# Kernel tuning notes

Hardware: AMD Instinct MI355X
Metric: run time of the kernel (lower is better)

The kernel has to match this reference:

```python
import jax, jax.numpy as jnp
import numpy as np

B = 262144      # batch
DIN = 100       # input covariate dim (cfg_density[0][0])
H = 64          # hidden dim
G = 10          # num_grid -> density output dim G+1
NH = 5          # number of dosage-bucket heads in Multi_head


def setup_inputs() -> dict:
    key = jax.random.key(0)
    ks = jax.random.split(key, 16)
    s = 0.05
    return {
        "dosage": jax.random.uniform(ks[0], (B,), dtype=jnp.float32),
        "x": jax.random.normal(ks[1], (B, DIN), dtype=jnp.float32),
        # density feature MLP (two Linear+ReLU layers)
        "dW0": jax.random.normal(ks[2], (DIN, H), dtype=jnp.float32) * s,
        "db0": jax.random.normal(ks[3], (H,), dtype=jnp.float32) * s,
        "dW1": jax.random.normal(ks[4], (H, H), dtype=jnp.float32) * s,
        "db1": jax.random.normal(ks[5], (H,), dtype=jnp.float32) * s,
        # Density_Block: Linear(H -> G+1) then softmax + grid interpolation
        "dbW": jax.random.normal(ks[6], (H, G + 1), dtype=jnp.float32) * s,
        "dbB": jax.random.normal(ks[7], (G + 1,), dtype=jnp.float32) * s,
        # Multi_head: 5 structurally identical heads, params stacked on axis 0
        # layer0: Treat_Linear(64 -> 64, relu, istreat=1)
        "W0": jax.random.normal(ks[8], (NH, H, H), dtype=jnp.float32) * s,
        "tw0": jax.random.normal(ks[9], (NH, H), dtype=jnp.float32) * s,
        "b0": jax.random.normal(ks[10], (NH, H), dtype=jnp.float32) * s,
        # layer1 (last): Treat_Linear(64 -> 1, no act, istreat=1)
        "W1": jax.random.normal(ks[11], (NH, H, 1), dtype=jnp.float32) * s,
        "tw1": jax.random.normal(ks[12], (NH, 1), dtype=jnp.float32) * s,
        "b1": jax.random.normal(ks[13], (NH, 1), dtype=jnp.float32) * s,
    }


def reference(dosage, x, dW0, db0, dW1, db1, dbW, dbB, W0, tw0, b0, W1, tw1, b1):
    # hidden feature MLP
    hidden = jax.nn.relu(x @ dW0 + db0)
    hidden = jax.nn.relu(hidden @ dW1 + db1)            # [B, H]

    # ---- Density_Block: softmax over grid, dual gather + linear interpolation
    p = jax.nn.softmax(hidden @ dbW + dbB, axis=1)      # [B, G+1]
    tB = dosage * G
    U = jnp.ceil(tB)
    inter = 1.0 - (U - tB)                              # fractional position in cell
    Ui = U.astype(jnp.int32)
    Li = Ui - 1
    Li = Li + (Li < 0).astype(jnp.int32)                # clamp L=-1 -> 0
    pL = jnp.take_along_axis(p, Li[:, None], axis=1)[:, 0]
    pU = jnp.take_along_axis(p, Ui[:, None], axis=1)[:, 0]
    g = pL + (pU - pL) * inter                          # [B]

    # ---- Multi_head: 5 heads on dosage buckets [0,.2),[.2,.4),...,[.8,1.)
    t = dosage
    # layer0: out = feat @ W + t * tw + b, relu; compute all heads, select later
    h0 = jax.nn.relu(
        jnp.einsum('bi,hio->bho', hidden, W0)
        + t[:, None, None] * tw0[None]
        + b0[None]
    )                                                   # [B, NH, H]
    # last layer: no activation
    out1 = (jnp.einsum('bho,hoj->bhj', h0, W1)
            + t[:, None, None] * tw1[None]
            + b1[None])                                 # [B, NH, 1]
    bucket = jnp.clip(jnp.floor(t * NH).astype(jnp.int32), 0, NH - 1)
    Q = jnp.take_along_axis(out1, bucket[:, None, None], axis=1)[:, 0, :]  # [B, 1]
    return g, Q
```

## Files before the change

kernel.cpp:

```cpp
#include <hip/hip_runtime.h>

typedef __attribute__((ext_vector_type(8))) short  short8;
typedef __attribute__((ext_vector_type(4))) float  floatx4;
typedef __attribute__((ext_vector_type(4))) int    intx4;

constexpr int DIN = 100;
constexpr int H   = 64;
constexpr int G   = 10;
constexpr int NH  = 5;
constexpr int MWG = 128;
constexpr int HP  = 72;
constexpr int PBP = 20;

constexpr int NF_DW0 = 16, NF_DW1 = 8, NF_DBW = 2;
constexpr int NF_LIN = NF_DW0 + NF_DW1 + NF_DBW;
constexpr int NF_TOT = NF_LIN + 40;

__device__ __forceinline__ unsigned short f2bf_rne(float f) {
    union { float f; unsigned u; } v{f};
    unsigned r = v.u + 0x7FFF + ((v.u >> 16) & 1);
    return (unsigned short)(r >> 16);
}

__device__ __forceinline__ short8 pack8(const float* f) {
    intx4 p;
    #pragma unroll
    for (int j = 0; j < 4; ++j) {
        unsigned a = __float_as_uint(f[2 * j])     + 0x8000u;
        unsigned b = __float_as_uint(f[2 * j + 1]) + 0x8000u;
        p[j] = (int)((b & 0xFFFF0000u) | (a >> 16));
    }
    union { intx4 i; short8 s; } u; u.i = p;
    return u.s;
}

__device__ __forceinline__ unsigned pack2bf(float a, float b) {
    unsigned ua = __float_as_uint(a) + 0x8000u;
    unsigned ub = __float_as_uint(b) + 0x8000u;
    return (ua >> 16) | (ub & 0xFFFF0000u);
}

__device__ __forceinline__ short8 ldfrag(const unsigned short* __restrict__ ws,
                                         int f, int lane) {
    return *(const short8*)(ws + (size_t)(f * 64 + lane) * 8);
}

__global__ __launch_bounds__(64) void pack_kernel(
    const float* __restrict__ dW0, const float* __restrict__ dW1,
    const float* __restrict__ dbW, const float* __restrict__ W0,
    unsigned short* __restrict__ ws)
{
    const int f = blockIdx.x;
    const int lane = threadIdx.x;
    const int q = lane >> 4, cl = lane & 15;
    float v[8];
    if (f < NF_DW0) {
        int c = f >> 2, g = f & 3;
        #pragma unroll
        for (int j = 0; j < 8; ++j) {
            int k = c * 32 + q * 8 + j, n = g * 16 + cl;
            v[j] = (k < DIN) ? dW0[k * H + n] : 0.0f;
        }
    } else if (f < NF_DW0 + NF_DW1) {
        int r = f - NF_DW0; int c = r >> 2, g = r & 3;
        #pragma unroll
        for (int j = 0; j < 8; ++j) {
            int k = c * 32 + q * 8 + j, n = g * 16 + cl;
            v[j] = dW1[k * H + n];
        }
    } else if (f < NF_LIN) {
        int c = f - (NF_DW0 + NF_DW1);
        #pragma unroll
        for (int j = 0; j < 8; ++j) {
            int k = c * 32 + q * 8 + j, n = cl;
            v[j] = (n <= G) ? dbW[k * (G + 1) + n] : 0.0f;
        }
    } else {
        int r = f - NF_LIN; int h = r >> 3; r &= 7; int c = r >> 2, g = r & 3;
        #pragma unroll
        for (int j = 0; j < 8; ++j) {
            int k = c * 32 + q * 8 + j, n = g * 16 + cl;
            v[j] = W0[(h * H + k) * H + n];
        }
    }
    short8 s;
    #pragma unroll
    for (int j = 0; j < 8; ++j) s[j] = (short)f2bf_rne(v[j]);
    *(short8*)(ws + (size_t)(f * 64 + lane) * 8) = s;
}

__global__ __launch_bounds__(256, 3) void drnet_mfma(
    const float* __restrict__ dosage, const float* __restrict__ x,
    const float* __restrict__ db0, const float* __restrict__ db1,
    const float* __restrict__ dbB,
    const float* __restrict__ tw0, const float* __restrict__ b0,
    const float* __restrict__ W1, const float* __restrict__ tw1,
    const float* __restrict__ b1,
    const unsigned short* __restrict__ wsfrag,
    float* __restrict__ outg, float* __restrict__ outq)
{
    __shared__ unsigned short hbuf[MWG * HP];
    __shared__ float          pbuf[4][16][PBP];
    __shared__ int            perm[MWG];
    __shared__ float          tbuf[MWG];
    __shared__ unsigned char  bkbuf[MWG];
    __shared__ float          qbuf[MWG];
    __shared__ int            hist[NH];
    __shared__ int            offs[NH];

    const int tid  = threadIdx.x;
    const int wave = tid >> 6, lane = tid & 63;
    const int q = lane >> 4, cl = lane & 15;
    const int rowbase = blockIdx.x * MWG + wave * 32;
    unsigned short* hb = hbuf + wave * 32 * HP;

    if (tid < NH) hist[tid] = 0;
    __syncthreads();
    {
        float t8[2][4];
        int   bk8[2][4];
        #pragma unroll
        for (int mt = 0; mt < 2; ++mt) {
            floatx4 tv = *(const floatx4*)(dosage + rowbase + mt * 16 + 4 * q);
            #pragma unroll
            for (int r = 0; r < 4; ++r) {
                float t = tv[r];
                t8[mt][r] = t;
                int bk = (int)floorf(t * (float)NH);
                bk8[mt][r] = min(max(bk, 0), NH - 1);
            }
        }
        if (cl == 0) {
            #pragma unroll
            for (int mt = 0; mt < 2; ++mt)
                #pragma unroll
                for (int r = 0; r < 4; ++r)
                    atomicAdd(&hist[bk8[mt][r]], 1);
        }
        __syncthreads();
        if (tid == 0) {
            int a = 0;
            #pragma unroll
            for (int h = 0; h < NH; ++h) { offs[h] = a; a += hist[h]; }
        }
        __syncthreads();
        if (cl == 0) {
            #pragma unroll
            for (int mt = 0; mt < 2; ++mt)
                #pragma unroll
                for (int r = 0; r < 4; ++r) {
                    const int bk  = bk8[mt][r];
                    const int pos = atomicAdd(&offs[bk], 1);
                    perm[pos]  = wave * 32 + mt * 16 + 4 * q + r;
                    tbuf[pos]  = t8[mt][r];
                    bkbuf[pos] = (unsigned char)bk;
                }
        }
    }

    #pragma unroll 1
    for (int mt = 0; mt < 2; ++mt) {
        short8 a1[4];
        const float* xr = x + (size_t)(rowbase + mt * 16 + cl) * DIN;
        #pragma unroll
        for (int cch = 0; cch < 4; ++cch) {
            float f[8];
            if (cch < 3) {
                floatx4 u0 = *(const floatx4*)(xr + cch * 32 + q * 8);
                floatx4 u1 = *(const floatx4*)(xr + cch * 32 + q * 8 + 4);
                f[0]=u0.x; f[1]=u0.y; f[2]=u0.z; f[3]=u0.w;
                f[4]=u1.x; f[5]=u1.y; f[6]=u1.z; f[7]=u1.w;
            } else {
                if (q == 0) {
                    floatx4 u0 = *(const floatx4*)(xr + 96);
                    f[0]=u0.x; f[1]=u0.y; f[2]=u0.z; f[3]=u0.w;
                    f[4]=f[5]=f[6]=f[7]=0.0f;
                } else {
                    #pragma unroll
                    for (int j = 0; j < 8; ++j) f[j] = 0.0f;
                }
            }
            a1[cch] = pack8(f);
        }
        floatx4 acc[4];
        #pragma unroll
        for (int g = 0; g < 4; ++g) acc[g] = (floatx4)0.0f;
        #pragma unroll
        for (int cch = 0; cch < 4; ++cch)
            #pragma unroll
            for (int g = 0; g < 4; ++g) {
                short8 bf = ldfrag(wsfrag, cch * 4 + g, lane);
                acc[g] = __builtin_amdgcn_mfma_f32_16x16x32_bf16(bf, a1[cch], acc[g], 0, 0, 0);
            }
        #pragma unroll
        for (int g = 0; g < 4; ++g) {
            floatx4 bias = *(const floatx4*)(db0 + g * 16 + 4 * q);
            float v0 = fmaxf(acc[g][0] + bias[0], 0.0f);
            float v1 = fmaxf(acc[g][1] + bias[1], 0.0f);
            float v2 = fmaxf(acc[g][2] + bias[2], 0.0f);
            float v3 = fmaxf(acc[g][3] + bias[3], 0.0f);
            *(uint2*)(hb + (size_t)(mt * 16 + cl) * HP + g * 16 + 4 * q) =
                make_uint2(pack2bf(v0, v1), pack2bf(v2, v3));
        }
    }

    #pragma unroll 1
    for (int mt = 0; mt < 2; ++mt) {
        short8 a2[2];
        #pragma unroll
        for (int cch = 0; cch < 2; ++cch)
            a2[cch] = *(const short8*)(hb + (mt * 16 + cl) * HP + cch * 32 + q * 8);
        floatx4 acc[4];
        #pragma unroll
        for (int g = 0; g < 4; ++g) acc[g] = (floatx4)0.0f;
        #pragma unroll
        for (int cch = 0; cch < 2; ++cch)
            #pragma unroll
            for (int g = 0; g < 4; ++g) {
                short8 bf = ldfrag(wsfrag, NF_DW0 + cch * 4 + g, lane);
                acc[g] = __builtin_amdgcn_mfma_f32_16x16x32_bf16(bf, a2[cch], acc[g], 0, 0, 0);
            }
        #pragma unroll
        for (int g = 0; g < 4; ++g) {
            floatx4 bias = *(const floatx4*)(db1 + g * 16 + 4 * q);
            float v0 = fmaxf(acc[g][0] + bias[0], 0.0f);
            float v1 = fmaxf(acc[g][1] + bias[1], 0.0f);
            float v2 = fmaxf(acc[g][2] + bias[2], 0.0f);
            float v3 = fmaxf(acc[g][3] + bias[3], 0.0f);
            *(uint2*)(hb + (size_t)(mt * 16 + cl) * HP + g * 16 + 4 * q) =
                make_uint2(pack2bf(v0, v1), pack2bf(v2, v3));
        }
    }

    short8 af[2][2];
    #pragma unroll
    for (int mt = 0; mt < 2; ++mt)
        #pragma unroll
        for (int cch = 0; cch < 2; ++cch)
            af[mt][cch] = *(const short8*)(hb + (mt * 16 + cl) * HP + cch * 32 + q * 8);

    {
        floatx4 accd[2];
        accd[0] = (floatx4)0.0f; accd[1] = (floatx4)0.0f;
        #pragma unroll
        for (int cch = 0; cch < 2; ++cch) {
            short8 bf = ldfrag(wsfrag, NF_DW0 + NF_DW1 + cch, lane);
            #pragma unroll
            for (int mt = 0; mt < 2; ++mt)
                accd[mt] = __builtin_amdgcn_mfma_f32_16x16x32_bf16(bf, af[mt][cch], accd[mt], 0, 0, 0);
        }
        #pragma unroll
        for (int mt = 0; mt < 2; ++mt) {
            floatx4 ev;
            float sp = 0.0f;
            #pragma unroll
            for (int r = 0; r < 4; ++r) {
                const int gd = 4 * q + r;
                float e = (gd <= G) ? __expf(accd[mt][r] + dbB[gd]) : 0.0f;
                ev[r] = e;
                sp += e;
            }
            float s = sp;
            s += __shfl_xor(s, 16); s += __shfl_xor(s, 32);
            *(floatx4*)(&pbuf[wave][cl][4 * q]) = ev;
            const float t  = dosage[rowbase + mt * 16 + cl];
            const float tB = t * (float)G;
            const float U  = ceilf(tB);
            const float inter = 1.0f - (U - tB);
            int Ui = (int)U; int Li = Ui - 1; if (Li < 0) Li = 0;
            const float pL = pbuf[wave][cl][Li];
            const float pU = pbuf[wave][cl][Ui];
            if (q == 0)
                outg[rowbase + mt * 16 + cl] = (pL + (pU - pL) * inter) / s;
        }
    }

    __syncthreads();
    #pragma unroll 1
    for (int mt = 0; mt < 2; ++mt) {
        const int base = (wave * 2 + mt) * 16;
        const int prow = perm[base + cl];
        short8 ag[2];
        ag[0] = *(const short8*)(hbuf + prow * HP + q * 8);
        ag[1] = *(const short8*)(hbuf + prow * HP + 32 + q * 8);
        const float tme  = tbuf[base + cl];
        const int   bkme = bkbuf[base + cl];
        const int   blo  = bkbuf[base], bhi = bkbuf[base + 15];
        float qp = 0.0f;
        #pragma unroll 1
        for (int h = blo; h <= bhi; ++h) {
            floatx4 acch[4];
            #pragma unroll
            for (int g = 0; g < 4; ++g) acch[g] = (floatx4)0.0f;
            #pragma unroll
            for (int cch = 0; cch < 2; ++cch)
                #pragma unroll
                for (int g = 0; g < 4; ++g) {
                    short8 bf = ldfrag(wsfrag, NF_LIN + h * 8 + cch * 4 + g, lane);
                    acch[g] = __builtin_amdgcn_mfma_f32_16x16x32_bf16(bf, ag[cch], acch[g], 0, 0, 0);
                }
            if (bkme == h) {
                #pragma unroll
                for (int g = 0; g < 4; ++g) {
                    const int off = h * H + g * 16 + 4 * q;
                    floatx4 tw0v = *(const floatx4*)(tw0 + off);
                    floatx4 b0v  = *(const floatx4*)(b0  + off);
                    floatx4 w1v  = *(const floatx4*)(W1  + off);
                    #pragma unroll
                    for (int r = 0; r < 4; ++r)
                        qp += fmaxf(acch[g][r] + tme * tw0v[r] + b0v[r], 0.0f) * w1v[r];
                }
            }
        }
        qp += __shfl_xor(qp, 16); qp += __shfl_xor(qp, 32);
        if (q == 0)
            qbuf[prow] = qp + tme * tw1[bkme] + b1[bkme];
    }

    __syncthreads();
    if (tid < MWG / 4) {
        floatx4 v = *(const floatx4*)(qbuf + tid * 4);
        *(floatx4*)(outq + blockIdx.x * MWG + tid * 4) = v;
    }
}

extern "C" void kernel_launch(void* const* d_in, const int* in_sizes, int n_in,
                              void* d_out, int out_size, void* d_ws, size_t ws_size,
                              hipStream_t stream) {
    const float* dosage = (const float*)d_in[0];
    const float* x      = (const float*)d_in[1];
    const float* dW0    = (const float*)d_in[2];
    const float* db0    = (const float*)d_in[3];
    const float* dW1    = (const float*)d_in[4];
    const float* db1    = (const float*)d_in[5];
    const float* dbW    = (const float*)d_in[6];
    const float* dbB    = (const float*)d_in[7];
    const float* W0     = (const float*)d_in[8];
    const float* tw0    = (const float*)d_in[9];
    const float* b0     = (const float*)d_in[10];
    const float* W1     = (const float*)d_in[11];
    const float* tw1    = (const float*)d_in[12];
    const float* b1     = (const float*)d_in[13];

    const int Btot = in_sizes[0];
    float* outg = (float*)d_out;
    float* outq = outg + Btot;
    unsigned short* ws = (unsigned short*)d_ws;

    pack_kernel<<<NF_TOT, 64, 0, stream>>>(dW0, dW1, dbW, W0, ws);
    drnet_mfma<<<Btot / MWG, 256, 0, stream>>>(dosage, x, db0, db1, dbB,
                                               tw0, b0, W1, tw1, b1,
                                               ws, outg, outq);
}
```

Before: 204.7 us.

## Prefetch x and dosage before the histogram barriers and interleave both M-tiles

Global loads of x rows and dosage are issued at the top of the kernel, before the bucket-sort histogram. The barriers there are replaced with LDS-only waits (lgkmcnt) so those loads stay in flight across the sort. The two 16-row tiles in each GEMM layer are fully unrolled and their MFMAs interleaved, sharing each weight fragment load and giving more independent MFMA chains. The cost is much higher register pressure from 14 floatx4 of x per lane plus doubled accumulators, which could lower occupancy or cause spills.

```diff
diff --git a/kernel.cpp b/kernel.cpp
--- a/kernel.cpp
+++ b/kernel.cpp
@@ -43,6 +43,12 @@
 __device__ __forceinline__ short8 ldfrag(const unsigned short* __restrict__ ws,
                                          int f, int lane) {
     return *(const short8*)(ws + (size_t)(f * 64 + lane) * 8);
+}
+
+__device__ __forceinline__ void bar_lgkm() {
+    asm volatile("s_waitcnt lgkmcnt(0)" ::: "memory");
+    __builtin_amdgcn_s_barrier();
+    asm volatile("" ::: "memory");
 }
 
 __global__ __launch_bounds__(64) void pack_kernel(
@@ -114,22 +120,36 @@
     const int rowbase = blockIdx.x * MWG + wave * 32;
     unsigned short* hb = hbuf + wave * 32 * HP;
 
+    floatx4 tvs[2];
+    #pragma unroll
+    for (int mt = 0; mt < 2; ++mt)
+        tvs[mt] = *(const floatx4*)(dosage + rowbase + mt * 16 + 4 * q);
+    floatx4 xv[2][7];
+    #pragma unroll
+    for (int mt = 0; mt < 2; ++mt) {
+        const float* xr = x + (size_t)(rowbase + mt * 16 + cl) * DIN;
+        #pragma unroll
+        for (int cch = 0; cch < 3; ++cch) {
+            xv[mt][2 * cch]     = *(const floatx4*)(xr + cch * 32 + q * 8);
+            xv[mt][2 * cch + 1] = *(const floatx4*)(xr + cch * 32 + q * 8 + 4);
+        }
+        xv[mt][6] = (q == 0) ? *(const floatx4*)(xr + 96) : (floatx4)0.0f;
+    }
+
     if (tid < NH) hist[tid] = 0;
-    __syncthreads();
+    bar_lgkm();
     {
         float t8[2][4];
         int   bk8[2][4];
         #pragma unroll
-        for (int mt = 0; mt < 2; ++mt) {
-            floatx4 tv = *(const floatx4*)(dosage + rowbase + mt * 16 + 4 * q);
+        for (int mt = 0; mt < 2; ++mt)
             #pragma unroll
             for (int r = 0; r < 4; ++r) {
-                float t = tv[r];
+                float t = tvs[mt][r];
                 t8[mt][r] = t;
                 int bk = (int)floorf(t * (float)NH);
                 bk8[mt][r] = min(max(bk, 0), NH - 1);
             }
-        }
         if (cl == 0) {
             #pragma unroll
             for (int mt = 0; mt < 2; ++mt)
@@ -137,13 +157,13 @@
                 for (int r = 0; r < 4; ++r)
                     atomicAdd(&hist[bk8[mt][r]], 1);
         }
-        __syncthreads();
+        bar_lgkm();
         if (tid == 0) {
             int a = 0;
             #pragma unroll
             for (int h = 0; h < NH; ++h) { offs[h] = a; a += hist[h]; }
         }
-        __syncthreads();
+        bar_lgkm();
         if (cl == 0) {
             #pragma unroll
             for (int mt = 0; mt < 2; ++mt)
@@ -158,88 +178,100 @@
         }
     }
 
-    #pragma unroll 1
-    for (int mt = 0; mt < 2; ++mt) {
-        short8 a1[4];
-        const float* xr = x + (size_t)(rowbase + mt * 16 + cl) * DIN;
-        #pragma unroll
-        for (int cch = 0; cch < 4; ++cch) {
-            float f[8];
-            if (cch < 3) {
-                floatx4 u0 = *(const floatx4*)(xr + cch * 32 + q * 8);
-                floatx4 u1 = *(const floatx4*)(xr + cch * 32 + q * 8 + 4);
-                f[0]=u0.x; f[1]=u0.y; f[2]=u0.z; f[3]=u0.w;
-                f[4]=u1.x; f[5]=u1.y; f[6]=u1.z; f[7]=u1.w;
-            } else {
-                if (q == 0) {
-                    floatx4 u0 = *(const floatx4*)(xr + 96);
-                    f[0]=u0.x; f[1]=u0.y; f[2]=u0.z; f[3]=u0.w;
-                    f[4]=f[5]=f[6]=f[7]=0.0f;
+    {
+        short8 a1[2][4];
+        #pragma unroll
+        for (int mt = 0; mt < 2; ++mt)
+            #pragma unroll
+            for (int cch = 0; cch < 4; ++cch) {
+                float f[8];
+                if (cch < 3) {
+                    #pragma unroll
+                    for (int j = 0; j < 4; ++j) {
+                        f[j]     = xv[mt][2 * cch][j];
+                        f[4 + j] = xv[mt][2 * cch + 1][j];
+                    }
                 } else {
                     #pragma unroll
-                    for (int j = 0; j < 8; ++j) f[j] = 0.0f;
+                    for (int j = 0; j < 4; ++j) {
+                        f[j]     = xv[mt][6][j];
+                        f[4 + j] = 0.0f;
+                    }
                 }
-            }
-            a1[cch] = pack8(f);
-        }
-        floatx4 acc[4];
-        #pragma unroll
-        for (int g = 0; g < 4; ++g) acc[g] = (floatx4)0.0f;
+                a1[mt][cch] = pack8(f);
+            }
+        floatx4 acc[2][4];
+        #pragma unroll
+        for (int mt = 0; mt < 2; ++mt)
+            #pragma unroll
+            for (int g = 0; g < 4; ++g) acc[mt][g] = (floatx4)0.0f;
         #pragma unroll
         for (int cch = 0; cch < 4; ++cch)
             #pragma unroll
             for (int g = 0; g < 4; ++g) {
                 short8 bf = ldfrag(wsfrag, cch * 4 + g, lane);
-                acc[g] = __builtin_amdgcn_mfma_f32_16x16x32_bf16(bf, a1[cch], acc[g], 0, 0, 0);
-            }
-        #pragma unroll
-        for (int g = 0; g < 4; ++g) {
-            floatx4 bias = *(const floatx4*)(db0 + g * 16 + 4 * q);
-            float v0 = fmaxf(acc[g][0] + bias[0], 0.0f);
-            float v1 = fmaxf(acc[g][1] + bias[1], 0.0f);
-            float v2 = fmaxf(acc[g][2] + bias[2], 0.0f);
-            float v3 = fmaxf(acc[g][3] + bias[3], 0.0f);
-            *(uint2*)(hb + (size_t)(mt * 16 + cl) * HP + g * 16 + 4 * q) =
-                make_uint2(pack2bf(v0, v1), pack2bf(v2, v3));
-        }
-    }
-
-    #pragma unroll 1
-    for (int mt = 0; mt < 2; ++mt) {
-        short8 a2[2];
-        #pragma unroll
-        for (int cch = 0; cch < 2; ++cch)
-            a2[cch] = *(const short8*)(hb + (mt * 16 + cl) * HP + cch * 32 + q * 8);
-        floatx4 acc[4];
-        #pragma unroll
-        for (int g = 0; g < 4; ++g) acc[g] = (floatx4)0.0f;
+                acc[0][g] = __builtin_amdgcn_mfma_f32_16x16x32_bf16(bf, a1[0][cch], acc[0][g], 0, 0, 0);
+                acc[1][g] = __builtin_amdgcn_mfma_f32_16x16x32_bf16(bf, a1[1][cch], acc[1][g], 0, 0, 0);
+            }
+        #pragma unroll
+        for (int mt = 0; mt < 2; ++mt)
+            #pragma unroll
+            for (int g = 0; g < 4; ++g) {
+                floatx4 bias = *(const floatx4*)(db0 + g * 16 + 4 * q);
+                float v0 = fmaxf(acc[mt][g][0] + bias[0], 0.0f);
+                float v1 = fmaxf(acc[mt][g][1] + bias[1], 0.0f);
+                float v2 = fmaxf(acc[mt][g][2] + bias[2], 0.0f);
+                float v3 = fmaxf(acc[mt][g][3] + bias[3], 0.0f);
+                *(uint2*)(hb + (size_t)(mt * 16 + cl) * HP + g * 16 + 4 * q) =
+                    make_uint2(pack2bf(v0, v1), pack2bf(v2, v3));
+            }
+    }
+
+    {
+        short8 a2[2][2];
+        #pragma unroll
+        for (int mt = 0; mt < 2; ++mt)
+            #pragma unroll
+            for (int cch = 0; cch < 2; ++cch)
+                a2[mt][cch] = *(const short8*)(hb + (mt * 16 + cl) * HP + cch * 32 + q * 8);
+        floatx4 acc[2][4];
+        #pragma unroll
+        for (int mt = 0; mt < 2; ++mt)
+            #pragma unroll
+            for (int g = 0; g < 4; ++g) acc[mt][g] = (floatx4)0.0f;
         #pragma unroll
         for (int cch = 0; cch < 2; ++cch)
             #pragma unroll
             for (int g = 0; g < 4; ++g) {
                 short8 bf = ldfrag(wsfrag, NF_DW0 + cch * 4 + g, lane);
-                acc[g] = __builtin_amdgcn_mfma_f32_16x16x32_bf16(bf, a2[cch], acc[g], 0, 0, 0);
-            }
-        #pragma unroll
-        for (int g = 0; g < 4; ++g) {
-            floatx4 bias = *(const floatx4*)(db1 + g * 16 + 4 * q);
-            float v0 = fmaxf(acc[g][0] + bias[0], 0.0f);
-            float v1 = fmaxf(acc[g][1] + bias[1], 0.0f);
-            float v2 = fmaxf(acc[g][2] + bias[2], 0.0f);
-            float v3 = fmaxf(acc[g][3] + bias[3], 0.0f);
-            *(uint2*)(hb + (size_t)(mt * 16 + cl) * HP + g * 16 + 4 * q) =
-                make_uint2(pack2bf(v0, v1), pack2bf(v2, v3));
-        }
-    }
-
-    short8 af[2][2];
-    #pragma unroll
-    for (int mt = 0; mt < 2; ++mt)
-        #pragma unroll
-        for (int cch = 0; cch < 2; ++cch)
-            af[mt][cch] = *(const short8*)(hb + (mt * 16 + cl) * HP + cch * 32 + q * 8);
-
-    {
+                acc[0][g] = __builtin_amdgcn_mfma_f32_16x16x32_bf16(bf, a2[0][cch], acc[0][g], 0, 0, 0);
+                acc[1][g] = __builtin_amdgcn_mfma_f32_16x16x32_bf16(bf, a2[1][cch], acc[1][g], 0, 0, 0);
+            }
+        #pragma unroll
+        for (int mt = 0; mt < 2; ++mt)
+            #pragma unroll
+            for (int g = 0; g < 4; ++g) {
+                floatx4 bias = *(const floatx4*)(db1 + g * 16 + 4 * q);
+                float v0 = fmaxf(acc[mt][g][0] + bias[0], 0.0f);
+                float v1 = fmaxf(acc[mt][g][1] + bias[1], 0.0f);
+                float v2 = fmaxf(acc[mt][g][2] + bias[2], 0.0f);
+                float v3 = fmaxf(acc[mt][g][3] + bias[3], 0.0f);
+                *(uint2*)(hb + (size_t)(mt * 16 + cl) * HP + g * 16 + 4 * q) =
+                    make_uint2(pack2bf(v0, v1), pack2bf(v2, v3));
+            }
+    }
+
+    {
+        float tden[2];
+        #pragma unroll
+        for (int mt = 0; mt < 2; ++mt)
+            tden[mt] = dosage[rowbase + mt * 16 + cl];
+        short8 af[2][2];
+        #pragma unroll
+        for (int mt = 0; mt < 2; ++mt)
+            #pragma unroll
+            for (int cch = 0; cch < 2; ++cch)
+                af[mt][cch] = *(const short8*)(hb + (mt * 16 + cl) * HP + cch * 32 + q * 8);
         floatx4 accd[2];
         accd[0] = (floatx4)0.0f; accd[1] = (floatx4)0.0f;
         #pragma unroll
@@ -263,7 +295,7 @@
             float s = sp;
             s += __shfl_xor(s, 16); s += __shfl_xor(s, 32);
             *(floatx4*)(&pbuf[wave][cl][4 * q]) = ev;
-            const float t  = dosage[rowbase + mt * 16 + cl];
+            const float t  = tden[mt];
             const float tB = t * (float)G;
             const float U  = ceilf(tB);
             const float inter = 1.0f - (U - tB);
@@ -276,45 +308,53 @@
     }
 
     __syncthreads();
-    #pragma unroll 1
-    for (int mt = 0; mt < 2; ++mt) {
-        const int base = (wave * 2 + mt) * 16;
-        const int prow = perm[base + cl];
-        short8 ag[2];
-        ag[0] = *(const short8*)(hbuf + prow * HP + q * 8);
-        ag[1] = *(const short8*)(hbuf + prow * HP + 32 + q * 8);
-        const float tme  = tbuf[base + cl];
-        const int   bkme = bkbuf[base + cl];
-        const int   blo  = bkbuf[base], bhi = bkbuf[base + 15];
-        float qp = 0.0f;
-        #pragma unroll 1
-        for (int h = blo; h <= bhi; ++h) {
-            floatx4 acch[4];
-            #pragma unroll
-            for (int g = 0; g < 4; ++g) acch[g] = (floatx4)0.0f;
-            #pragma unroll
-            for (int cch = 0; cch < 2; ++cch)
+    {
+        short8 ag[2][2];
+        int    prow[2], bkme[2], blo[2], bhi[2];
+        float  tme[2];
+        #pragma unroll
+        for (int mt = 0; mt < 2; ++mt) {
+            const int base = (wave * 2 + mt) * 16;
+            prow[mt] = perm[base + cl];
+            ag[mt][0] = *(const short8*)(hbuf + prow[mt] * HP + q * 8);
+            ag[mt][1] = *(const short8*)(hbuf + prow[mt] * HP + 32 + q * 8);
+            tme[mt]  = tbuf[base + cl];
+            bkme[mt] = bkbuf[base + cl];
+            blo[mt]  = bkbuf[base];
+            bhi[mt]  = bkbuf[base + 15];
+        }
+        #pragma unroll
+        for (int mt = 0; mt < 2; ++mt) {
+            float qp = 0.0f;
+            #pragma unroll 1
+            for (int h = blo[mt]; h <= bhi[mt]; ++h) {
+                floatx4 acch[4];
                 #pragma unroll
-                for (int g = 0; g < 4; ++g) {
-                    short8 bf = ldfrag(wsfrag, NF_LIN + h * 8 + cch * 4 + g, lane);
-                    acch[g] = __builtin_amdgcn_mfma_f32_16x16x32_bf16(bf, ag[cch], acch[g], 0, 0, 0);
+                for (int g = 0; g < 4; ++g) acch[g] = (floatx4)0.0f;
+                #pragma unroll
+                for (int cch = 0; cch < 2; ++cch)
+                    #pragma unroll
+                    for (int g = 0; g < 4; ++g) {
+                        short8 bf = ldfrag(wsfrag, NF_LIN + h * 8 + cch * 4 + g, lane);
+                        acch[g] = __builtin_amdgcn_mfma_f32_16x16x32_bf16(bf, ag[mt][cch], acch[g], 0, 0, 0);
+                    }
+                if (bkme[mt] == h) {
+                    #pragma unroll
+                    for (int g = 0; g < 4; ++g) {
+                        const int off = h * H + g * 16 + 4 * q;
+                        floatx4 tw0v = *(const floatx4*)(tw0 + off);
+                        floatx4 b0v  = *(const floatx4*)(b0  + off);
+                        floatx4 w1v  = *(const floatx4*)(W1  + off);
+                        #pragma unroll
+                        for (int r = 0; r < 4; ++r)
+                            qp += fmaxf(acch[g][r] + tme[mt] * tw0v[r] + b0v[r], 0.0f) * w1v[r];
+                    }
                 }
-            if (bkme == h) {
-                #pragma unroll
-                for (int g = 0; g < 4; ++g) {
-                    const int off = h * H + g * 16 + 4 * q;
-                    floatx4 tw0v = *(const floatx4*)(tw0 + off);
-                    floatx4 b0v  = *(const floatx4*)(b0  + off);
-                    floatx4 w1v  = *(const floatx4*)(W1  + off);
-                    #pragma unroll
-                    for (int r = 0; r < 4; ++r)
-                        qp += fmaxf(acch[g][r] + tme * tw0v[r] + b0v[r], 0.0f) * w1v[r];
-                }
-            }
-        }
-        qp += __shfl_xor(qp, 16); qp += __shfl_xor(qp, 32);
-        if (q == 0)
-            qbuf[prow] = qp + tme * tw1[bkme] + b1[bkme];
+            }
+            qp += __shfl_xor(qp, 16); qp += __shfl_xor(qp, 32);
+            if (q == 0)
+                qbuf[prow[mt]] = qp + tme[mt] * tw1[bkme[mt]] + b1[bkme[mt]];
+        }
     }
 
     __syncthreads();
```

New measurement: 198.7 us. 3.0% less time.
